# Kernel optimization log

Measured on AMD Instinct MI355X. Metric: run time of the kernel, lower is better.

The kernel has to match this reference:

```python
import jax, jax.numpy as jnp
import numpy as np

H = 768
FF = 3072
NH = 12
DH = H // NH


def setup_inputs() -> dict:
    key = jax.random.key(0)
    ks = jax.random.split(key, 16)
    s = 0.02
    return {
        "latent": jax.random.normal(ks[0], (2, 2048, H), jnp.float32),
        "ln1_w": jnp.ones((H,), jnp.float32),
        "ln1_b": jnp.zeros((H,), jnp.float32),
        "Wq": jax.random.normal(ks[1], (H, H), jnp.float32) * s,
        "bq": jnp.zeros((H,), jnp.float32),
        "Wk": jax.random.normal(ks[2], (H, H), jnp.float32) * s,
        "bk": jnp.zeros((H,), jnp.float32),
        "Wv": jax.random.normal(ks[3], (H, H), jnp.float32) * s,
        "bv": jnp.zeros((H,), jnp.float32),
        "Wo": jax.random.normal(ks[4], (H, H), jnp.float32) * s,
        "bo": jnp.zeros((H,), jnp.float32),
        "ln2_w": jnp.ones((H,), jnp.float32),
        "ln2_b": jnp.zeros((H,), jnp.float32),
        "W1": jax.random.normal(ks[5], (H, FF), jnp.float32) * s,
        "b1": jnp.zeros((FF,), jnp.float32),
        "W2": jax.random.normal(ks[6], (FF, H), jnp.float32) * s,
        "b2": jnp.zeros((H,), jnp.float32),
    }


def _layernorm(x, w, b, eps=1e-6):
    mu = jnp.mean(x, axis=-1, keepdims=True)
    var = jnp.mean(jnp.square(x - mu), axis=-1, keepdims=True)
    return (x - mu) * jax.lax.rsqrt(var + eps) * w + b


def _split_heads(x):  # [B,S,H] -> [B,NH,S,DH]
    B, S, _ = x.shape
    return x.reshape(B, S, NH, DH).transpose(0, 2, 1, 3)


def reference(latent, ln1_w, ln1_b, Wq, bq, Wk, bk, Wv, bv, Wo, bo,
              ln2_w, ln2_b, W1, b1, W2, b2):
    B, S, _ = latent.shape
    # MHSA (dropouts are p=0.0 / eval mode -> identity)
    nx = _layernorm(latent, ln1_w, ln1_b)
    q = _split_heads(nx @ Wq + bq)
    k = _split_heads(nx @ Wk + bk)
    v = _split_heads(nx @ Wv + bv)
    scores = jnp.einsum('bhqd,bhkd->bhqk', q, k) / jnp.sqrt(jnp.float32(DH))
    attn = jax.nn.softmax(scores, axis=-1)
    ctx = jnp.einsum('bhqk,bhkd->bhqd', attn, v)
    ctx = ctx.transpose(0, 2, 1, 3).reshape(B, S, H)
    latent = latent + (ctx @ Wo + bo)
    # FFN (exact erf GELU as in torch nn.GELU default)
    nx = _layernorm(latent, ln2_w, ln2_b)
    h = jax.nn.gelu(nx @ W1 + b1, approximate=False)
    latent = latent + (h @ W2 + b2)
    return latent
```

## Files before the change

### kernel.cpp

```cpp
#include <hip/hip_runtime.h>

#define H 768
#define FF 3072
#define NH 12
#define DH 64
#define SEQ 2048
#define MTOK 4096

typedef __attribute__((ext_vector_type(8))) short short8;
typedef __attribute__((ext_vector_type(4))) float f32x4;
typedef __attribute__((ext_vector_type(2))) unsigned int uint2v;


__device__ __forceinline__ f32x4 mfma16(short8 a, short8 b, f32x4 c) {
  return __builtin_amdgcn_mfma_f32_16x16x32_bf16(a, b, c, 0, 0, 0);
}

__device__ __forceinline__ unsigned short f2bf(float f) {
  union { float f; unsigned int u; } c; c.f = f;
  unsigned int u = c.u;
  u += 0x7fffu + ((u >> 16) & 1u);
  return (unsigned short)(u >> 16);
}
__device__ __forceinline__ float bf2f(unsigned short s) {
  union { unsigned int u; float f; } c; c.u = ((unsigned int)s) << 16;
  return c.f;
}
__device__ __forceinline__ unsigned int pk2bf(float lo, float hi) {
  return (unsigned int)f2bf(lo) | ((unsigned int)f2bf(hi) << 16);
}
__device__ __forceinline__ unsigned int pktrunc(float lo, float hi) {
  union { float f; unsigned int u; } a, b; a.f = hi; b.f = lo;
  return __builtin_amdgcn_perm(a.u, b.u, 0x07060302u);
}

__device__ __forceinline__ void gld16(const unsigned short* g, unsigned short* l) {
  __builtin_amdgcn_global_load_lds(
      (const __attribute__((address_space(1))) void*)g,
      (__attribute__((address_space(3))) void*)l, 16, 0, 0);
}

__device__ __forceinline__ void ln_row(const float* __restrict__ xr, int row,
                                       const float* __restrict__ w,
                                       const float* __restrict__ b,
                                       unsigned short* __restrict__ out,
                                       int lane) {
  const float4* xv = (const float4*)xr;
  const float4* wv = (const float4*)w;
  const float4* bv = (const float4*)b;
  float4 v[3];
  float s = 0.f, ss = 0.f;
#pragma unroll
  for (int j = 0; j < 3; ++j) {
    v[j] = xv[lane + j * 64];
    s += v[j].x + v[j].y + v[j].z + v[j].w;
    ss += v[j].x * v[j].x + v[j].y * v[j].y + v[j].z * v[j].z + v[j].w * v[j].w;
  }
#pragma unroll
  for (int off = 32; off > 0; off >>= 1) {
    s += __shfl_xor(s, off);
    ss += __shfl_xor(ss, off);
  }
  float mu = s * (1.0f / H);
  float var = ss * (1.0f / H) - mu * mu;
  float rs = rsqrtf(var + 1e-6f);
  unsigned short* orow = out + (size_t)(row >> 4) * (24 * 512) + (row & 15) * 32;
#pragma unroll
  for (int j = 0; j < 3; ++j) {
    int c0 = lane * 4 + j * 256;
    float4 wj = wv[lane + j * 64];
    float4 bj = bv[lane + j * 64];
    float a0 = (v[j].x - mu) * rs * wj.x + bj.x;
    float a1 = (v[j].y - mu) * rs * wj.y + bj.y;
    float a2 = (v[j].z - mu) * rs * wj.z + bj.z;
    float a3 = (v[j].w - mu) * rs * wj.w + bj.w;
    int g = c0 >> 5;
    int swc = (c0 & 31) ^ ((row & 3) << 3);
    uint2 pk;
    pk.x = pk2bf(a0, a1);
    pk.y = pk2bf(a2, a3);
    *(uint2*)(orow + (size_t)g * 512 + swc) = pk;
  }
}

__global__ __launch_bounds__(256) void prep_kernel(
    const float* __restrict__ Wq, const float* __restrict__ Wk,
    const float* __restrict__ Wv, const float* __restrict__ Wo,
    const float* __restrict__ W1, const float* __restrict__ W2,
    unsigned short* __restrict__ WqkvT, unsigned short* __restrict__ WoT,
    unsigned short* __restrict__ W1T, unsigned short* __restrict__ W2T,
    const float* __restrict__ latent, const float* __restrict__ ln1_w,
    const float* __restrict__ ln1_b, unsigned short* __restrict__ nx) {
  int bid = blockIdx.x;
  int tid = threadIdx.x;
  if (bid >= 1728) {
    int wave = tid >> 6, lane = tid & 63;
    int row = (bid - 1728) * 4 + wave;
    ln_row(latent + (size_t)row * H, row, ln1_w, ln1_b, nx, lane);
    return;
  }
  const float* in; unsigned short* out; int K, N, t0;
  if (bid < 432) {
    K = 768; N = 768;
    int sub = bid / 144; t0 = bid % 144;
    in = (sub == 0) ? Wq : (sub == 1) ? Wk : Wv;
    out = WqkvT + (size_t)sub * 768 * 768;
  } else if (bid < 576) { in = Wo; out = WoT; K = 768;  N = 768;  t0 = bid - 432; }
  else if (bid < 1152)  { in = W1; out = W1T; K = 768;  N = 3072; t0 = bid - 576; }
  else                  { in = W2; out = W2T; K = 3072; N = 768;  t0 = bid - 1152; }

  __shared__ float tile[2][32][33];
  int nb = N >> 5;
  int n0 = (t0 % nb) << 5;
  int kc0 = (t0 / nb) << 7;
  int tx = tid & 31, ty = tid >> 5;
  int KT5 = K >> 5;
#pragma unroll
  for (int kk = 0; kk < 4; ++kk) {
    int k0 = kc0 + kk * 32;
    int bsel = kk & 1;
#pragma unroll
    for (int yy = 0; yy < 4; ++yy)
      tile[bsel][ty + yy * 8][tx] = in[(size_t)(k0 + ty + yy * 8) * N + n0 + tx];
    __syncthreads();
#pragma unroll
    for (int yy = 0; yy < 4; ++yy) {
      int n = n0 + ty + yy * 8;
      out[(size_t)((n >> 4) * KT5 + (k0 >> 5)) * 512 + (n & 15) * 32
          + (tx ^ ((n & 3) << 3))]
          = f2bf(tile[bsel][tx][ty + yy * 8]);
    }
  }
}

__global__ __launch_bounds__(256) void ln_kernel(const float* __restrict__ x,
                                                 const float* __restrict__ w,
                                                 const float* __restrict__ b,
                                                 unsigned short* __restrict__ out) {
  int wave = threadIdx.x >> 6, lane = threadIdx.x & 63;
  int row = blockIdx.x * 4 + wave;
  ln_row(x + (size_t)row * H, row, w, b, out, lane);
}

enum { MODE_QKV = 0, MODE_RESID = 1, MODE_GELU = 2 };

template <int MODE>
__global__ __launch_bounds__(256) void gemm128(
    const unsigned short* __restrict__ A,
    const unsigned short* __restrict__ Bt,
    int M, int N, int K,
    const float* __restrict__ bias0,
    const float* __restrict__ bias1,
    const float* __restrict__ bias2,
    unsigned short* __restrict__ out_q,
    unsigned short* __restrict__ out_k,
    unsigned short* __restrict__ out_vT,
    unsigned short* __restrict__ out_bf)
{
  const int mb = M >> 7;
  int m0 = (blockIdx.x % mb) << 7;
  int n0 = (blockIdx.x / mb) << 7;
  int tid = threadIdx.x;
  int wave = tid >> 6, lane = tid & 63;
  int quad = lane >> 4, l16 = lane & 15;
  int wm = (wave & 1) << 6;
  int wn = (wave >> 1) << 6;
  int KT = K >> 5;
  const size_t TS = (size_t)KT * 512;
  int swq = (quad ^ (l16 & 3)) << 3;

  __shared__ __align__(16) unsigned short As[2][128 * 32];
  __shared__ __align__(16) unsigned short Bs[2][128 * 32];

  f32x4 acc[4][4];
#pragma unroll
  for (int i = 0; i < 4; ++i)
#pragma unroll
    for (int j = 0; j < 4; ++j) acc[i][j] = (f32x4){0.f, 0.f, 0.f, 0.f};

  const unsigned short* gA = A + (size_t)((m0 >> 4) + wave * 2) * TS + lane * 8;
  const unsigned short* gB = Bt + (size_t)((n0 >> 4) + wave * 2) * TS + lane * 8;
  unsigned short* lA0 = &As[0][(wave * 32) * 32];
  unsigned short* lA1 = &As[0][(wave * 32 + 16) * 32];
  unsigned short* lB0 = &Bs[0][(wave * 32) * 32];
  unsigned short* lB1 = &Bs[0][(wave * 32 + 16) * 32];
  const int CH = 128 * 32;

  for (int ktb = 0; ktb < KT; ktb += 2) {
#pragma unroll
    for (int kc = 0; kc < 2; ++kc) {
      gld16(gA + (size_t)(ktb + kc) * 512,      lA0 + kc * CH);
      gld16(gA + TS + (size_t)(ktb + kc) * 512, lA1 + kc * CH);
      gld16(gB + (size_t)(ktb + kc) * 512,      lB0 + kc * CH);
      gld16(gB + TS + (size_t)(ktb + kc) * 512, lB1 + kc * CH);
    }
    __syncthreads();
#pragma unroll
    for (int kc = 0; kc < 2; ++kc) {
      short8 af[4], bfr[4];
#pragma unroll
      for (int t = 0; t < 4; ++t)
        af[t] = *(const short8*)(&As[kc][(wm + t * 16 + l16) * 32 + swq]);
#pragma unroll
      for (int t = 0; t < 4; ++t)
        bfr[t] = *(const short8*)(&Bs[kc][(wn + t * 16 + l16) * 32 + swq]);
#pragma unroll
      for (int i = 0; i < 4; ++i)
#pragma unroll
        for (int j = 0; j < 4; ++j)
          acc[i][j] = mfma16(af[i], bfr[j], acc[i][j]);
    }
    __syncthreads();
  }

#pragma unroll
  for (int mt = 0; mt < 4; ++mt)
#pragma unroll
    for (int nt = 0; nt < 4; ++nt) {
      f32x4 c = acc[mt][nt];
      int m = m0 + wm + mt * 16 + quad * 4;
      int n = n0 + wn + nt * 16 + l16;
      if (MODE == MODE_QKV) {
        int bb = m >> 11, sIdx = m & 2047;
        if (n < 768) {
          float bs = bias0[n];
          int hh = n >> 6, d = n & 63;
          unsigned short* dst = out_q + (((size_t)(bb * NH + hh)) * SEQ + sIdx) * DH + d;
#pragma unroll
          for (int r = 0; r < 4; ++r) dst[r * DH] = f2bf(c[r] + bs);
        } else if (n < 1536) {
          int nn = n - 768;
          float bs = bias1[nn];
          int hh = nn >> 6, d = nn & 63;
          size_t base = (size_t)(bb * NH + hh) * (SEQ * DH)
                      + (size_t)(sIdx >> 5) * 2048 + ((sIdx >> 4) & 1) * 1024
                      + (d >> 5) * 512 + (sIdx & 15) * 32 + (d & 31);
#pragma unroll
          for (int r = 0; r < 4; ++r) out_k[base + r * 32] = f2bf(c[r] + bs);
        } else {
          int nn = n - 1536;
          float bs = bias2[nn];
          int hh = nn >> 6, d = nn & 63;
          int k5 = sIdx & 31;
          int sa = (k5 & 0x11) | ((k5 & 0x6) << 1) | ((k5 >> 2) & 0x2);
          size_t cb = (size_t)(bb * NH + hh) * (SEQ * DH)
                    + (size_t)(sIdx >> 5) * 2048 + (d >> 4) * 512
                    + (d & 15) * 8 + (size_t)(sa >> 3) * 128;
          *(unsigned int*)(out_vT + cb + (sa & 7))       = pk2bf(c[0] + bs, c[1] + bs);
          *(unsigned int*)(out_vT + cb + ((sa & 7) | 4)) = pk2bf(c[2] + bs, c[3] + bs);
        }
      } else {
        float bs = bias0[n];
        int mtile = ((m0 + wm) >> 4) + mt;
        unsigned short* opb = out_bf + (size_t)(mtile * (N >> 5) + (n >> 5)) * 512
                              + quad * 4 * 32;
#pragma unroll
        for (int r = 0; r < 4; ++r) {
          float t = c[r] + bs;
          opb[r * 32 + ((n & 31) ^ ((r & 3) << 3))]
              = f2bf(0.5f * t * (1.0f + erff(t * 0.70710678118654752f)));
        }
      }
    }
}

template <int TAG>
__global__ __launch_bounds__(256) void gemm64r(
    const unsigned short* __restrict__ A,
    const unsigned short* __restrict__ Bt,
    int M, int N, int K,
    const float* __restrict__ bias0,
    const float* __restrict__ resid,
    float* __restrict__ out_f)
{
  const int mb = M >> 6;
  int m0 = (blockIdx.x % mb) << 6;
  int n0 = (blockIdx.x / mb) << 6;
  int tid = threadIdx.x;
  int wave = tid >> 6, lane = tid & 63;
  int quad = lane >> 4, l16 = lane & 15;
  int wm = (wave & 1) << 5;
  int wn = (wave >> 1) << 5;
  int KT = K >> 5;
  const size_t TS = (size_t)KT * 512;
  int swq = (quad ^ (l16 & 3)) << 3;

  __shared__ __align__(16) unsigned short As[4][64 * 32];
  __shared__ __align__(16) unsigned short Bs[4][64 * 32];

  f32x4 acc[2][2];
#pragma unroll
  for (int i = 0; i < 2; ++i)
#pragma unroll
    for (int j = 0; j < 2; ++j) acc[i][j] = (f32x4){0.f, 0.f, 0.f, 0.f};

  const unsigned short* gA = A + (size_t)((m0 >> 4) + wave) * TS + lane * 8;
  const unsigned short* gB = Bt + (size_t)((n0 >> 4) + wave) * TS + lane * 8;
  unsigned short* lA = &As[0][wave * 512];
  unsigned short* lB = &Bs[0][wave * 512];
  const int CH = 64 * 32;

  for (int ktb = 0; ktb < KT; ktb += 4) {
#pragma unroll
    for (int kc = 0; kc < 4; ++kc) {
      gld16(gA + (size_t)(ktb + kc) * 512, lA + kc * CH);
      gld16(gB + (size_t)(ktb + kc) * 512, lB + kc * CH);
    }
    __syncthreads();
#pragma unroll
    for (int kc = 0; kc < 4; ++kc) {
      short8 af[2], bfr[2];
#pragma unroll
      for (int t = 0; t < 2; ++t)
        af[t] = *(const short8*)(&As[kc][(wm + t * 16 + l16) * 32 + swq]);
#pragma unroll
      for (int t = 0; t < 2; ++t)
        bfr[t] = *(const short8*)(&Bs[kc][(wn + t * 16 + l16) * 32 + swq]);
#pragma unroll
      for (int i = 0; i < 2; ++i)
#pragma unroll
        for (int j = 0; j < 2; ++j)
          acc[i][j] = mfma16(af[i], bfr[j], acc[i][j]);
    }
    __syncthreads();
  }

#pragma unroll
  for (int mt = 0; mt < 2; ++mt)
#pragma unroll
    for (int nt = 0; nt < 2; ++nt) {
      f32x4 c = acc[mt][nt];
      int m = m0 + wm + mt * 16 + quad * 4;
      int n = n0 + wn + nt * 16 + l16;
      float bs = bias0[n];
      const float* rp = resid + (size_t)m * N + n;
      float* op = out_f + (size_t)m * N + n;
#pragma unroll
      for (int r = 0; r < 4; ++r) op[(size_t)r * N] = rp[(size_t)r * N] + c[r] + bs;
    }
}

__global__ __launch_bounds__(256, 4) void flash_attn_kernel(
    const unsigned short* __restrict__ q,
    const unsigned short* __restrict__ k,
    const unsigned short* __restrict__ vT,
    unsigned short* __restrict__ ctx)
{
  const float CEXP = 0.18033688011112042f;
  int bh = blockIdx.x % 24;
  int qblk = blockIdx.x / 24;
  int b = bh / NH, h = bh % NH;
  int tid = threadIdx.x;
  int wave = tid >> 6, lane = tid & 63;
  int quad = lane >> 4, l16 = lane & 15;
  int qbase = qblk << 5;

  const unsigned short* qp = q + ((size_t)bh * SEQ + qbase) * DH;
  const unsigned short* kbh = k + (size_t)bh * (SEQ * DH);
  const unsigned short* vbh = vT + (size_t)bh * (SEQ * DH);

  short8 qf00 = *(const short8*)(qp + l16 * DH + quad * 8);
  short8 qf01 = *(const short8*)(qp + l16 * DH + 32 + quad * 8);
  short8 qf10 = *(const short8*)(qp + (16 + l16) * DH + quad * 8);
  short8 qf11 = *(const short8*)(qp + (16 + l16) * DH + 32 + quad * 8);

  const short ONE = (short)0x3F80;
  short8 ones = (short8){ONE, ONE, ONE, ONE, ONE, ONE, ONE, ONE};

  f32x4 oacc[2][4];
  f32x4 lacc[2];
#pragma unroll
  for (int t = 0; t < 2; ++t) {
    lacc[t] = (f32x4){0.f, 0.f, 0.f, 0.f};
#pragma unroll
    for (int dt = 0; dt < 4; ++dt) oacc[t][dt] = (f32x4){0.f, 0.f, 0.f, 0.f};
  }

  int klin = (l16 * 4 + quad) * 8;
  int vlin = (quad * 16 + l16) * 8;

  int keylo = wave << 9;
  for (int key0 = keylo; key0 < keylo + 512; key0 += 32) {
    int cbase = (key0 >> 5) * 2048;
    short8 ka0 = *(const short8*)(kbh + cbase + klin);
    short8 ka1 = *(const short8*)(kbh + cbase + 512 + klin);
    short8 kb0 = *(const short8*)(kbh + cbase + 1024 + klin);
    short8 kb1 = *(const short8*)(kbh + cbase + 1536 + klin);
    short8 vf0 = *(const short8*)(vbh + cbase + 0 * 512 + vlin);
    short8 vf1 = *(const short8*)(vbh + cbase + 1 * 512 + vlin);
    short8 vf2 = *(const short8*)(vbh + cbase + 2 * 512 + vlin);
    short8 vf3 = *(const short8*)(vbh + cbase + 3 * 512 + vlin);

#pragma unroll
    for (int t = 0; t < 2; ++t) {
      short8 q0 = t ? qf10 : qf00;
      short8 q1 = t ? qf11 : qf01;
      f32x4 s0 = (f32x4){0.f, 0.f, 0.f, 0.f};
      f32x4 s1 = (f32x4){0.f, 0.f, 0.f, 0.f};
      s0 = mfma16(ka0, q0, s0);
      s0 = mfma16(ka1, q1, s0);
      s1 = mfma16(kb0, q0, s1);
      s1 = mfma16(kb1, q1, s1);

      f32x4 p0, p1;
#pragma unroll
      for (int r = 0; r < 4; ++r) {
        p0[r] = __builtin_amdgcn_exp2f(s0[r] * CEXP);
        p1[r] = __builtin_amdgcn_exp2f(s1[r] * CEXP);
      }

      unsigned int d00 = pktrunc(p0[0], p0[1]);
      unsigned int d01 = pktrunc(p0[2], p0[3]);
      unsigned int d10 = pktrunc(p1[0], p1[1]);
      unsigned int d11 = pktrunc(p1[2], p1[3]);

      uint2v rA = __builtin_amdgcn_permlane32_swap(d00, d10, false, false);
      uint2v rB = __builtin_amdgcn_permlane32_swap(d01, d11, false, false);
      union { short8 s; unsigned int i[4]; } pf;
      pf.i[0] = rA[0];
      pf.i[1] = rA[1];
      pf.i[2] = rB[0];
      pf.i[3] = rB[1];

      oacc[t][0] = mfma16(vf0, pf.s, oacc[t][0]);
      oacc[t][1] = mfma16(vf1, pf.s, oacc[t][1]);
      oacc[t][2] = mfma16(vf2, pf.s, oacc[t][2]);
      oacc[t][3] = mfma16(vf3, pf.s, oacc[t][3]);
      lacc[t]    = mfma16(ones, pf.s, lacc[t]);
    }
  }

  __shared__ float lbuf[4][2][16];
  __shared__ uint2 obuf[4][2][4][64];

  if (lane < 16) {
    lbuf[wave][0][lane] = lacc[0][0];
    lbuf[wave][1][lane] = lacc[1][0];
  }
#pragma unroll
  for (int t = 0; t < 2; ++t)
#pragma unroll
    for (int dt = 0; dt < 4; ++dt) {
      uint2 pk;
      pk.x = pk2bf(oacc[t][dt][0], oacc[t][dt][1]);
      pk.y = pk2bf(oacc[t][dt][2], oacc[t][dt][3]);
      obuf[wave][t][dt][lane] = pk;
    }
  __syncthreads();

#pragma unroll
  for (int pp = 0; pp < 2; ++pp) {
    int pi = wave * 2 + pp;
    int t = pi >> 2, dt = pi & 3;
    f32x4 sum = (f32x4){0.f, 0.f, 0.f, 0.f};
#pragma unroll
    for (int w = 0; w < 4; ++w) {
      uint2 pk = obuf[w][t][dt][lane];
      sum[0] += bf2f((unsigned short)(pk.x & 0xffff));
      sum[1] += bf2f((unsigned short)(pk.x >> 16));
      sum[2] += bf2f((unsigned short)(pk.y & 0xffff));
      sum[3] += bf2f((unsigned short)(pk.y >> 16));
    }
    float lstar = lbuf[0][t][l16] + lbuf[1][t][l16] + lbuf[2][t][l16] + lbuf[3][t][l16];
    float rinv = 1.0f / lstar;
    uint2 res;
    res.x = pk2bf(sum[0] * rinv, sum[1] * rinv);
    res.y = pk2bf(sum[2] * rinv, sum[3] * rinv);
    int colsw = (((dt & 1) * 16 + quad * 4)) ^ ((l16 & 3) << 3);
    unsigned short* crow = ctx
        + ((size_t)((b * SEQ + qbase + t * 16) >> 4) * 24 + h * 2 + (dt >> 1)) * 512
        + l16 * 32 + colsw;
    *(uint2*)crow = res;
  }
}

extern "C" void kernel_launch(void* const* d_in, const int* in_sizes, int n_in,
                              void* d_out, int out_size, void* d_ws, size_t ws_size,
                              hipStream_t stream) {
  const float* latent = (const float*)d_in[0];
  const float* ln1_w = (const float*)d_in[1];
  const float* ln1_b = (const float*)d_in[2];
  const float* Wq = (const float*)d_in[3];
  const float* bq = (const float*)d_in[4];
  const float* Wk = (const float*)d_in[5];
  const float* bk = (const float*)d_in[6];
  const float* Wv = (const float*)d_in[7];
  const float* bv = (const float*)d_in[8];
  const float* Wo = (const float*)d_in[9];
  const float* bo = (const float*)d_in[10];
  const float* ln2_w = (const float*)d_in[11];
  const float* ln2_b = (const float*)d_in[12];
  const float* W1 = (const float*)d_in[13];
  const float* b1 = (const float*)d_in[14];
  const float* W2 = (const float*)d_in[15];
  const float* b2 = (const float*)d_in[16];
  float* out = (float*)d_out;

  char* ws = (char*)d_ws;
  unsigned short* WqkvT = (unsigned short*)ws; ws += (size_t)2304 * 768 * 2;
  unsigned short* WoT   = (unsigned short*)ws; ws += (size_t)768 * 768 * 2;
  unsigned short* W1T   = (unsigned short*)ws; ws += (size_t)3072 * 768 * 2;
  unsigned short* W2T   = (unsigned short*)ws; ws += (size_t)768 * 3072 * 2;
  unsigned short* nx    = (unsigned short*)ws; ws += (size_t)MTOK * H * 2;
  unsigned short* nx2   = (unsigned short*)ws; ws += (size_t)MTOK * H * 2;
  unsigned short* qb    = (unsigned short*)ws; ws += (size_t)MTOK * H * 2;
  unsigned short* kb    = (unsigned short*)ws; ws += (size_t)MTOK * H * 2;
  unsigned short* vTb   = (unsigned short*)ws; ws += (size_t)MTOK * H * 2;
  unsigned short* ctx   = (unsigned short*)ws; ws += (size_t)MTOK * H * 2;
  unsigned short* hbuf  = (unsigned short*)ws; ws += (size_t)MTOK * FF * 2;
  float* x1             = (float*)ws;          ws += (size_t)MTOK * H * 4;

  prep_kernel<<<1728 + MTOK / 4, 256, 0, stream>>>(
      Wq, Wk, Wv, Wo, W1, W2, WqkvT, WoT, W1T, W2T,
      latent, ln1_w, ln1_b, nx);

  gemm128<MODE_QKV><<<32 * 18, 256, 0, stream>>>(
      nx, WqkvT, MTOK, 2304, 768, bq, bk, bv,
      qb, kb, vTb, nullptr);

  flash_attn_kernel<<<24 * 64, 256, 0, stream>>>(qb, kb, vTb, ctx);

  gemm64r<0><<<64 * 12, 256, 0, stream>>>(
      ctx, WoT, MTOK, 768, 768, bo, latent, x1);

  ln_kernel<<<MTOK / 4, 256, 0, stream>>>(x1, ln2_w, ln2_b, nx2);

  gemm128<MODE_GELU><<<32 * 24, 256, 0, stream>>>(
      nx2, W1T, MTOK, 3072, 768, b1, nullptr, nullptr,
      nullptr, nullptr, nullptr, hbuf);

  gemm64r<1><<<64 * 12, 256, 0, stream>>>(
      hbuf, W2T, MTOK, 768, 3072, b2, x1, out);
}
```

Measured before the change: 258.3 us.

## Double query tile per attention block and compute softmax denominators on VALU

Each flash-attention block now handles 64 query rows instead of 32, so every K/V fragment loaded from global memory is reused across four query sub-tiles. The grid is halved to match. The row-sum of exponentials moves from an extra MFMA against a ones vector to VALU adds followed by cross-lane shuffles. The trade-off is more accumulator registers and larger shared reduction buffers, which may lower occupancy under the launch bounds, and fewer blocks to spread across the GPU.

```diff
diff --git a/kernel.cpp b/kernel.cpp
--- a/kernel.cpp
+++ b/kernel.cpp
@@ -353,28 +353,25 @@
   int tid = threadIdx.x;
   int wave = tid >> 6, lane = tid & 63;
   int quad = lane >> 4, l16 = lane & 15;
-  int qbase = qblk << 5;
+  int qbase = qblk << 6;
 
   const unsigned short* qp = q + ((size_t)bh * SEQ + qbase) * DH;
   const unsigned short* kbh = k + (size_t)bh * (SEQ * DH);
   const unsigned short* vbh = vT + (size_t)bh * (SEQ * DH);
 
-  short8 qf00 = *(const short8*)(qp + l16 * DH + quad * 8);
-  short8 qf01 = *(const short8*)(qp + l16 * DH + 32 + quad * 8);
-  short8 qf10 = *(const short8*)(qp + (16 + l16) * DH + quad * 8);
-  short8 qf11 = *(const short8*)(qp + (16 + l16) * DH + 32 + quad * 8);
-
-  const short ONE = (short)0x3F80;
-  short8 ones = (short8){ONE, ONE, ONE, ONE, ONE, ONE, ONE, ONE};
-
-  f32x4 oacc[2][4];
-  f32x4 lacc[2];
-#pragma unroll
-  for (int t = 0; t < 2; ++t) {
-    lacc[t] = (f32x4){0.f, 0.f, 0.f, 0.f};
+  short8 qf0[4], qf1[4];
+#pragma unroll
+  for (int t = 0; t < 4; ++t) {
+    qf0[t] = *(const short8*)(qp + (t * 16 + l16) * DH + quad * 8);
+    qf1[t] = *(const short8*)(qp + (t * 16 + l16) * DH + 32 + quad * 8);
+  }
+
+  f32x4 oacc[4][4];
+  float L[4] = {0.f, 0.f, 0.f, 0.f};
+#pragma unroll
+  for (int t = 0; t < 4; ++t)
 #pragma unroll
     for (int dt = 0; dt < 4; ++dt) oacc[t][dt] = (f32x4){0.f, 0.f, 0.f, 0.f};
-  }
 
   int klin = (l16 * 4 + quad) * 8;
   int vlin = (quad * 16 + l16) * 8;
@@ -392,15 +389,13 @@
     short8 vf3 = *(const short8*)(vbh + cbase + 3 * 512 + vlin);
 
 #pragma unroll
-    for (int t = 0; t < 2; ++t) {
-      short8 q0 = t ? qf10 : qf00;
-      short8 q1 = t ? qf11 : qf01;
+    for (int t = 0; t < 4; ++t) {
       f32x4 s0 = (f32x4){0.f, 0.f, 0.f, 0.f};
       f32x4 s1 = (f32x4){0.f, 0.f, 0.f, 0.f};
-      s0 = mfma16(ka0, q0, s0);
-      s0 = mfma16(ka1, q1, s0);
-      s1 = mfma16(kb0, q0, s1);
-      s1 = mfma16(kb1, q1, s1);
+      s0 = mfma16(ka0, qf0[t], s0);
+      s0 = mfma16(ka1, qf1[t], s0);
+      s1 = mfma16(kb0, qf0[t], s1);
+      s1 = mfma16(kb1, qf1[t], s1);
 
       f32x4 p0, p1;
 #pragma unroll
@@ -408,6 +403,7 @@
         p0[r] = __builtin_amdgcn_exp2f(s0[r] * CEXP);
         p1[r] = __builtin_amdgcn_exp2f(s1[r] * CEXP);
       }
+      L[t] += (p0[0] + p0[1]) + (p0[2] + p0[3]) + (p1[0] + p1[1]) + (p1[2] + p1[3]);
 
       unsigned int d00 = pktrunc(p0[0], p0[1]);
       unsigned int d01 = pktrunc(p0[2], p0[3]);
@@ -426,19 +422,24 @@
       oacc[t][1] = mfma16(vf1, pf.s, oacc[t][1]);
       oacc[t][2] = mfma16(vf2, pf.s, oacc[t][2]);
       oacc[t][3] = mfma16(vf3, pf.s, oacc[t][3]);
-      lacc[t]    = mfma16(ones, pf.s, lacc[t]);
-    }
-  }
-
-  __shared__ float lbuf[4][2][16];
-  __shared__ uint2 obuf[4][2][4][64];
+    }
+  }
+
+#pragma unroll
+  for (int t = 0; t < 4; ++t) {
+    L[t] += __shfl_xor(L[t], 16);
+    L[t] += __shfl_xor(L[t], 32);
+  }
+
+  __shared__ float lbuf[4][4][16];
+  __shared__ uint2 obuf[4][4][4][64];
 
   if (lane < 16) {
-    lbuf[wave][0][lane] = lacc[0][0];
-    lbuf[wave][1][lane] = lacc[1][0];
-  }
-#pragma unroll
-  for (int t = 0; t < 2; ++t)
+#pragma unroll
+    for (int t = 0; t < 4; ++t) lbuf[wave][t][lane] = L[t];
+  }
+#pragma unroll
+  for (int t = 0; t < 4; ++t)
 #pragma unroll
     for (int dt = 0; dt < 4; ++dt) {
       uint2 pk;
@@ -449,9 +450,8 @@
   __syncthreads();
 
 #pragma unroll
-  for (int pp = 0; pp < 2; ++pp) {
-    int pi = wave * 2 + pp;
-    int t = pi >> 2, dt = pi & 3;
+  for (int pp = 0; pp < 4; ++pp) {
+    int t = pp, dt = wave;
     f32x4 sum = (f32x4){0.f, 0.f, 0.f, 0.f};
 #pragma unroll
     for (int w = 0; w < 4; ++w) {
@@ -518,7 +518,7 @@
       nx, WqkvT, MTOK, 2304, 768, bq, bk, bv,
       qb, kb, vTb, nullptr);
 
-  flash_attn_kernel<<<24 * 64, 256, 0, stream>>>(qb, kb, vTb, ctx);
+  flash_attn_kernel<<<24 * 32, 256, 0, stream>>>(qb, kb, vTb, ctx);
 
   gemm64r<0><<<64 * 12, 256, 0, stream>>>(
       ctx, WoT, MTOK, 768, 768, bo, latent, x1);
```

After: 314.8 us. 21.8% more time.
